# Optimization experiments

Hardware: AMD Instinct MI355X
Metric: run time of the kernel (lower is better)

The kernel has to match this reference:

```python
import jax, jax.numpy as jnp
import numpy as np

N, D_IN, D_OUT, E = 16384, 2048, 2048, 8


def setup_inputs() -> dict:
    key = jax.random.key(0)
    k1, k2, k3, k4 = jax.random.split(key, 4)
    x = jax.random.normal(k1, (N, D_IN), dtype=jnp.float32)
    idxs = jax.random.randint(k2, (N,), 0, E, dtype=jnp.int64)
    # nn.Linear params: weight [out, in], bias [out]; stacked over experts.
    W = jax.random.normal(k3, (E, D_OUT, D_IN), dtype=jnp.float32) * (1.0 / np.sqrt(D_IN))
    b = jax.random.normal(k4, (E, D_OUT), dtype=jnp.float32) * 0.01
    return {"x": x, "idxs": idxs, "W": W, "b": b}


def reference(x, idxs, W, b):
    # Hard-routed MoE: each token goes to exactly one expert's Linear, then ReLU.
    # Loop over the small fixed expert count; each iteration is one dense GEMM
    # over all tokens, combined with a per-token routing mask (equivalent math
    # to the original masked gather/scatter since every token matches exactly
    # one expert id in [0, E)).
    n_experts = W.shape[0]
    y = jnp.zeros((x.shape[0], W.shape[1]), dtype=x.dtype)
    for e in range(n_experts):
        mask = (idxs == e)[:, None]  # [N, 1]
        y_e = x @ W[e].T + b[e]      # [N, out]
        y = jnp.where(mask, y_e, y)
    return jax.nn.relu(y)
```

## Files before the change

kernel.cpp:

```cpp
#include <hip/hip_runtime.h>
#include <stdint.h>

#define N_TOK 16384
#define D_IN  2048
#define D_OUT 2048
#define NEXP  8

#define BM 128
#define BN 128
#define BK 32

typedef __attribute__((ext_vector_type(8))) short bf16x8;
typedef __attribute__((ext_vector_type(4))) float f32x4;
typedef __attribute__((ext_vector_type(4))) unsigned short u16x4;

static __device__ __forceinline__ unsigned short f2bf(float x) {
  unsigned u = __builtin_bit_cast(unsigned, x);
  u += 0x7FFFu + ((u >> 16) & 1u);
  return (unsigned short)(u >> 16);
}
static __device__ __forceinline__ float bf2f(unsigned short h) {
  unsigned u = ((unsigned)h) << 16;
  return __builtin_bit_cast(float, u);
}

__global__ void zero_cnt(int* cnt) {
  if (threadIdx.x < NEXP) cnt[threadIdx.x] = 0;
}

__global__ void route_kernel(const int* __restrict__ idxs, int* __restrict__ cnt,
                             int* __restrict__ bucket) {
  int t = blockIdx.x * blockDim.x + threadIdx.x;
  if (t < N_TOK) {
    int e = idxs[t];
    int slot = atomicAdd(&cnt[e], 1);
    bucket[e * N_TOK + slot] = t;
  }
}

__global__ void split_kernel(const float* __restrict__ in, unsigned short* __restrict__ hi,
                             unsigned short* __restrict__ lo, int n4) {
  int i = blockIdx.x * blockDim.x + threadIdx.x;
  int stride = gridDim.x * blockDim.x;
  const float4* in4 = (const float4*)in;
  for (; i < n4; i += stride) {
    float4 v = in4[i];
    float f[4] = {v.x, v.y, v.z, v.w};
    u16x4 h, l;
#pragma unroll
    for (int j = 0; j < 4; ++j) {
      unsigned short hh = f2bf(f[j]);
      h[j] = hh;
      l[j] = f2bf(f[j] - bf2f(hh));
    }
    *(u16x4*)(hi + (size_t)i * 4) = h;
    *(u16x4*)(lo + (size_t)i * 4) = l;
  }
}

#define GLD16(g, l)                                                                       \
  __builtin_amdgcn_global_load_lds((const __attribute__((address_space(1))) void*)(g),    \
                                   (__attribute__((address_space(3))) void*)(l), 16, 0, 0)

__global__ __launch_bounds__(256)
void moe_gemm(const unsigned short* __restrict__ xhi, const unsigned short* __restrict__ xlo,
              const unsigned short* __restrict__ whi, const unsigned short* __restrict__ wlo,
              const float* __restrict__ bias, const int* __restrict__ cnt,
              const int* __restrict__ bucket, float* __restrict__ out) {
  const int e = blockIdx.z;
  const int count = cnt[e];
  const int m0 = blockIdx.y * BM;
  if (m0 >= count) return;
  const int n0 = blockIdx.x * BN;

  __shared__ __align__(16) unsigned short sAh[BM * BK];
  __shared__ __align__(16) unsigned short sAl[BM * BK];
  __shared__ __align__(16) unsigned short sBh[BN * BK];
  __shared__ __align__(16) unsigned short sBl[BN * BK];
  __shared__ int rowtok[BM];

  const int tid = threadIdx.x;
  const int lane = tid & 63;
  const int wave = tid >> 6;

  if (tid < BM) {
    int r = m0 + tid;
    rowtok[tid] = bucket[e * N_TOK + (r < count ? r : count - 1)];
  }
  __syncthreads();

  const int s0 = tid;
  const int s1 = 256 + tid;
  const int row0 = s0 >> 2, seg0 = s0 & 3;
  const int row1 = s1 >> 2, seg1 = s1 & 3;
  const int tok0 = rowtok[row0];
  const int tok1 = rowtok[row1];
  const size_t aOff0 = (size_t)tok0 * D_IN + seg0 * 8;
  const size_t aOff1 = (size_t)tok1 * D_IN + seg1 * 8;
  const size_t bOff0 = (size_t)(n0 + row0) * D_IN + seg0 * 8;
  const size_t bOff1 = (size_t)(n0 + row1) * D_IN + seg1 * 8;
  const unsigned short* wBh = whi + (size_t)e * D_OUT * D_IN;
  const unsigned short* wBl = wlo + (size_t)e * D_OUT * D_IN;
  const int lb0 = wave * 1024;
  const int lb1 = 4096 + wave * 1024;

  f32x4 acc[4][4];
#pragma unroll
  for (int i = 0; i < 4; ++i)
#pragma unroll
    for (int j = 0; j < 4; ++j) acc[i][j] = (f32x4)0.0f;

  const int r16 = lane & 15;
  const int ko = (lane >> 4) * 8;
  const int wm = (wave >> 1) * 64;
  const int wn = (wave & 1) * 64;

  for (int kt = 0; kt < D_IN; kt += BK) {
    __syncthreads();
    GLD16(xhi + aOff0 + kt, (char*)sAh + lb0);
    GLD16(xhi + aOff1 + kt, (char*)sAh + lb1);
    GLD16(xlo + aOff0 + kt, (char*)sAl + lb0);
    GLD16(xlo + aOff1 + kt, (char*)sAl + lb1);
    GLD16(wBh + bOff0 + kt, (char*)sBh + lb0);
    GLD16(wBh + bOff1 + kt, (char*)sBh + lb1);
    GLD16(wBl + bOff0 + kt, (char*)sBl + lb0);
    GLD16(wBl + bOff1 + kt, (char*)sBl + lb1);
    __syncthreads();

    bf16x8 ah[4], al[4], bh[4], bl[4];
#pragma unroll
    for (int i = 0; i < 4; ++i) {
      ah[i] = *(const bf16x8*)&sAh[(wm + i * 16 + r16) * BK + ko];
      al[i] = *(const bf16x8*)&sAl[(wm + i * 16 + r16) * BK + ko];
      bh[i] = *(const bf16x8*)&sBh[(wn + i * 16 + r16) * BK + ko];
      bl[i] = *(const bf16x8*)&sBl[(wn + i * 16 + r16) * BK + ko];
    }
#pragma unroll
    for (int mi = 0; mi < 4; ++mi)
#pragma unroll
      for (int ni = 0; ni < 4; ++ni) {
        acc[mi][ni] = __builtin_amdgcn_mfma_f32_16x16x32_bf16(ah[mi], bh[ni], acc[mi][ni], 0, 0, 0);
        acc[mi][ni] = __builtin_amdgcn_mfma_f32_16x16x32_bf16(ah[mi], bl[ni], acc[mi][ni], 0, 0, 0);
        acc[mi][ni] = __builtin_amdgcn_mfma_f32_16x16x32_bf16(al[mi], bh[ni], acc[mi][ni], 0, 0, 0);
      }
  }

  const int rbase = (lane >> 4) * 4;
#pragma unroll
  for (int ni = 0; ni < 4; ++ni) {
    const int gn = n0 + wn + ni * 16 + r16;
    const float bv = bias[e * D_OUT + gn];
#pragma unroll
    for (int mi = 0; mi < 4; ++mi) {
#pragma unroll
      for (int i = 0; i < 4; ++i) {
        const int lr = wm + mi * 16 + rbase + i;
        if (m0 + lr < count) {
          const int tok = rowtok[lr];
          out[(size_t)tok * D_OUT + gn] = fmaxf(acc[mi][ni][i] + bv, 0.0f);
        }
      }
    }
  }
}

__global__ void fallback_kernel(const float* __restrict__ x, const int* __restrict__ idxs,
                                const float* __restrict__ W, const float* __restrict__ b,
                                float* __restrict__ out) {
  const int row = blockIdx.y;
  const int col = blockIdx.x * 256 + threadIdx.x;
  const int e = idxs[row];
  const float4* xr = (const float4*)(x + (size_t)row * D_IN);
  const float4* wr = (const float4*)(W + ((size_t)e * D_OUT + col) * D_IN);
  float acc = 0.f;
  for (int k = 0; k < D_IN / 4; ++k) {
    float4 a = xr[k], w = wr[k];
    acc += a.x * w.x + a.y * w.y + a.z * w.z + a.w * w.w;
  }
  out[(size_t)row * D_OUT + col] = fmaxf(acc + b[e * D_OUT + col], 0.0f);
}

extern "C" void kernel_launch(void* const* d_in, const int* in_sizes, int n_in,
                              void* d_out, int out_size, void* d_ws, size_t ws_size,
                              hipStream_t stream) {
  const float* x = (const float*)d_in[0];
  const int* idxs = (const int*)d_in[1];
  const float* W = (const float*)d_in[2];
  const float* b = (const float*)d_in[3];
  float* out = (float*)d_out;

  size_t off = 0;
  auto alloc = [&](size_t bytes) {
    void* p = (char*)d_ws + off;
    off += (bytes + 255) & ~(size_t)255;
    return p;
  };
  int* cnt = (int*)alloc(NEXP * sizeof(int));
  int* bucket = (int*)alloc((size_t)NEXP * N_TOK * sizeof(int));
  unsigned short* xhi = (unsigned short*)alloc((size_t)N_TOK * D_IN * 2);
  unsigned short* xlo = (unsigned short*)alloc((size_t)N_TOK * D_IN * 2);
  unsigned short* whi = (unsigned short*)alloc((size_t)NEXP * D_OUT * D_IN * 2);
  unsigned short* wlo = (unsigned short*)alloc((size_t)NEXP * D_OUT * D_IN * 2);

  if (off > ws_size) {
    dim3 g(D_OUT / 256, N_TOK, 1);
    fallback_kernel<<<g, 256, 0, stream>>>(x, idxs, W, b, out);
    return;
  }

  zero_cnt<<<1, 64, 0, stream>>>(cnt);
  route_kernel<<<(N_TOK + 255) / 256, 256, 0, stream>>>(idxs, cnt, bucket);

  const int n4x = N_TOK * D_IN / 4;
  const int n4w = NEXP * D_OUT * D_IN / 4;
  split_kernel<<<2048, 256, 0, stream>>>(x, xhi, xlo, n4x);
  split_kernel<<<2048, 256, 0, stream>>>(W, whi, wlo, n4w);

  dim3 grid(D_OUT / BN, (N_TOK + BM - 1) / BM, NEXP);
  moe_gemm<<<grid, 256, 0, stream>>>(xhi, xlo, whi, wlo, b, cnt, bucket, out);
}
```

Measured before the change: 931.5 us.

## Use 256x256 tiles with double-buffered swizzled LDS and interleaved MFMA scheduling

The grouped GEMM moves to 256x256 tiles on 8 waves, with a double-buffered 64KB-per-stage LDS ring. Global-to-LDS loads for the next K step are interleaved with four MFMA phases, separated by scheduling barriers and priority hints. An XOR swizzle on the LDS layout avoids bank conflicts, and the routing kernel now uses shared-memory histograms to cut global atomics. The larger tiles raise operand reuse and overlap memory with compute, at the cost of more padding waste per expert and lower occupancy from the 128KB of LDS per block.

Result: faster. 847.2 us (-9.0%).

```diff
diff --git a/kernel.cpp b/kernel.cpp
--- a/kernel.cpp
+++ b/kernel.cpp
@@ -6,9 +6,10 @@
 #define D_OUT 2048
 #define NEXP  8
 
-#define BM 128
-#define BN 128
+#define BM 256
+#define BN 256
 #define BK 32
+#define NKT (D_IN / BK)
 
 typedef __attribute__((ext_vector_type(8))) short bf16x8;
 typedef __attribute__((ext_vector_type(4))) float f32x4;
@@ -30,12 +31,20 @@
 
 __global__ void route_kernel(const int* __restrict__ idxs, int* __restrict__ cnt,
                              int* __restrict__ bucket) {
-  int t = blockIdx.x * blockDim.x + threadIdx.x;
-  if (t < N_TOK) {
-    int e = idxs[t];
-    int slot = atomicAdd(&cnt[e], 1);
-    bucket[e * N_TOK + slot] = t;
-  }
+  __shared__ int hist[NEXP];
+  __shared__ int base[NEXP];
+  __shared__ int pos[NEXP];
+  const int t = blockIdx.x * 256 + threadIdx.x;
+  if (threadIdx.x < NEXP) { hist[threadIdx.x] = 0; pos[threadIdx.x] = 0; }
+  __syncthreads();
+  const int e = idxs[t];
+  atomicAdd(&hist[e], 1);
+  __syncthreads();
+  if (threadIdx.x < NEXP)
+    base[threadIdx.x] = atomicAdd(&cnt[threadIdx.x], hist[threadIdx.x]);
+  __syncthreads();
+  const int r = atomicAdd(&pos[e], 1);
+  bucket[e * N_TOK + base[e] + r] = t;
 }
 
 __global__ void split_kernel(const float* __restrict__ in, unsigned short* __restrict__ hi,
@@ -58,11 +67,50 @@
   }
 }
 
-#define GLD16(g, l)                                                                       \
-  __builtin_amdgcn_global_load_lds((const __attribute__((address_space(1))) void*)(g),    \
+#define GLD16(g, l)                                                                    \
+  __builtin_amdgcn_global_load_lds((const __attribute__((address_space(1))) void*)(g), \
                                    (__attribute__((address_space(3))) void*)(l), 16, 0, 0)
-
-__global__ __launch_bounds__(256)
+#define SB() __builtin_amdgcn_sched_barrier(0)
+#define BAR() __builtin_amdgcn_s_barrier()
+
+template <int MH>
+static __device__ __forceinline__ void loadA(const char* rb, int wr, int off0,
+                                             bf16x8 (&afr)[4][2]) {
+#pragma unroll
+  for (int mf = 0; mf < 4; ++mf) {
+    const int ro = (wr * 128 + MH * 64 + mf * 16) * 128;
+    afr[mf][0] = *(const bf16x8*)(rb + ro + off0);
+    afr[mf][1] = *(const bf16x8*)(rb + ro + (off0 ^ 64));
+  }
+}
+
+template <int NH>
+static __device__ __forceinline__ void loadB(const char* rb, int wc, int off0,
+                                             bf16x8 (&bfr)[2][2]) {
+#pragma unroll
+  for (int nf = 0; nf < 2; ++nf) {
+    const int ro = 32768 + (wc * 64 + NH * 32 + nf * 16) * 128;
+    bfr[nf][0] = *(const bf16x8*)(rb + ro + off0);
+    bfr[nf][1] = *(const bf16x8*)(rb + ro + (off0 ^ 64));
+  }
+}
+
+template <int MH, int NH>
+static __device__ __forceinline__ void mfma24(bf16x8 (&afr)[4][2], bf16x8 (&bfr)[2][2],
+                                              f32x4 (&acc)[8][4]) {
+#pragma unroll
+  for (int mf = 0; mf < 4; ++mf)
+#pragma unroll
+    for (int nf = 0; nf < 2; ++nf) {
+      f32x4 a = acc[MH * 4 + mf][NH * 2 + nf];
+      a = __builtin_amdgcn_mfma_f32_16x16x32_bf16(afr[mf][0], bfr[nf][0], a, 0, 0, 0);
+      a = __builtin_amdgcn_mfma_f32_16x16x32_bf16(afr[mf][0], bfr[nf][1], a, 0, 0, 0);
+      a = __builtin_amdgcn_mfma_f32_16x16x32_bf16(afr[mf][1], bfr[nf][0], a, 0, 0, 0);
+      acc[MH * 4 + mf][NH * 2 + nf] = a;
+    }
+}
+
+__global__ __launch_bounds__(512, 2)
 void moe_gemm(const unsigned short* __restrict__ xhi, const unsigned short* __restrict__ xlo,
               const unsigned short* __restrict__ whi, const unsigned short* __restrict__ wlo,
               const float* __restrict__ bias, const int* __restrict__ cnt,
@@ -73,15 +121,14 @@
   if (m0 >= count) return;
   const int n0 = blockIdx.x * BN;
 
-  __shared__ __align__(16) unsigned short sAh[BM * BK];
-  __shared__ __align__(16) unsigned short sAl[BM * BK];
-  __shared__ __align__(16) unsigned short sBh[BN * BK];
-  __shared__ __align__(16) unsigned short sBl[BN * BK];
+  __shared__ __align__(16) char sbuf[2][65536];
   __shared__ int rowtok[BM];
 
   const int tid = threadIdx.x;
   const int lane = tid & 63;
-  const int wave = tid >> 6;
+  const int w = tid >> 6;
+  const int wr = w >> 2;
+  const int wc = w & 3;
 
   if (tid < BM) {
     int r = m0 + tid;
@@ -89,75 +136,90 @@
   }
   __syncthreads();
 
-  const int s0 = tid;
-  const int s1 = 256 + tid;
-  const int row0 = s0 >> 2, seg0 = s0 & 3;
-  const int row1 = s1 >> 2, seg1 = s1 & 3;
-  const int tok0 = rowtok[row0];
-  const int tok1 = rowtok[row1];
-  const size_t aOff0 = (size_t)tok0 * D_IN + seg0 * 8;
-  const size_t aOff1 = (size_t)tok1 * D_IN + seg1 * 8;
-  const size_t bOff0 = (size_t)(n0 + row0) * D_IN + seg0 * 8;
-  const size_t bOff1 = (size_t)(n0 + row1) * D_IN + seg1 * 8;
-  const unsigned short* wBh = whi + (size_t)e * D_OUT * D_IN;
-  const unsigned short* wBl = wlo + (size_t)e * D_OUT * D_IN;
-  const int lb0 = wave * 1024;
-  const int lb1 = 4096 + wave * 1024;
-
-  f32x4 acc[4][4];
-#pragma unroll
-  for (int i = 0; i < 4; ++i)
+  const unsigned short* whiE = whi + (size_t)e * D_OUT * D_IN;
+  const unsigned short* wloE = wlo + (size_t)e * D_OUT * D_IN;
+  const unsigned short* srcb[8];
+#pragma unroll
+  for (int q = 0; q < 8; ++q) {
+    const int r = (q & 3) * 64 + (tid >> 3);
+    const int c = (tid & 7) ^ ((tid >> 3) & 7);
+    const int half = c >> 2, kc = c & 3;
+    if (q < 4) {
+      const int tok = rowtok[r];
+      srcb[q] = (half ? xlo : xhi) + (size_t)tok * D_IN + kc * 8;
+    } else {
+      srcb[q] = (half ? wloE : whiE) + (size_t)(n0 + r) * D_IN + kc * 8;
+    }
+  }
+  const int dstoff = w * 1024;
+
+  const int off0 = (lane & 15) * 128 + (((lane >> 4) ^ (lane & 7)) * 16);
+
+  f32x4 acc[8][4];
+#pragma unroll
+  for (int i = 0; i < 8; ++i)
 #pragma unroll
     for (int j = 0; j < 4; ++j) acc[i][j] = (f32x4)0.0f;
+  bf16x8 afr[4][2], bfr[2][2];
+
+  {
+    char* wb = sbuf[0];
+#pragma unroll
+    for (int q = 0; q < 8; ++q) GLD16(srcb[q], wb + q * 8192 + dstoff);
+  }
+  asm volatile("s_waitcnt vmcnt(0)" ::: "memory");
+  SB(); BAR(); SB();
+
+  int cur = 0;
+  for (int i = 0; i < NKT; ++i) {
+    const char* rb = sbuf[cur];
+    char* wb = sbuf[cur ^ 1];
+    const int ktn = (i + 1) * BK;
+    const bool nx = (i + 1 < NKT);
+
+    loadA<0>(rb, wr, off0, afr);
+    loadB<0>(rb, wc, off0, bfr);
+    if (nx) { GLD16(srcb[0] + ktn, wb + 0 * 8192 + dstoff); GLD16(srcb[1] + ktn, wb + 1 * 8192 + dstoff); }
+    SB(); BAR(); SB();
+    __builtin_amdgcn_s_setprio(1); mfma24<0, 0>(afr, bfr, acc); __builtin_amdgcn_s_setprio(0);
+    SB(); BAR(); SB();
+
+    loadB<1>(rb, wc, off0, bfr);
+    if (nx) { GLD16(srcb[2] + ktn, wb + 2 * 8192 + dstoff); GLD16(srcb[3] + ktn, wb + 3 * 8192 + dstoff); }
+    SB(); BAR(); SB();
+    __builtin_amdgcn_s_setprio(1); mfma24<0, 1>(afr, bfr, acc); __builtin_amdgcn_s_setprio(0);
+    SB(); BAR(); SB();
+
+    loadA<1>(rb, wr, off0, afr);
+    loadB<0>(rb, wc, off0, bfr);
+    if (nx) { GLD16(srcb[4] + ktn, wb + 4 * 8192 + dstoff); GLD16(srcb[5] + ktn, wb + 5 * 8192 + dstoff); }
+    SB(); BAR(); SB();
+    __builtin_amdgcn_s_setprio(1); mfma24<1, 0>(afr, bfr, acc); __builtin_amdgcn_s_setprio(0);
+    SB(); BAR(); SB();
+
+    loadB<1>(rb, wc, off0, bfr);
+    if (nx) { GLD16(srcb[6] + ktn, wb + 6 * 8192 + dstoff); GLD16(srcb[7] + ktn, wb + 7 * 8192 + dstoff); }
+    SB(); BAR(); SB();
+    __builtin_amdgcn_s_setprio(1); mfma24<1, 1>(afr, bfr, acc); __builtin_amdgcn_s_setprio(0);
+    asm volatile("s_waitcnt vmcnt(0)" ::: "memory");
+    SB(); BAR(); SB();
+    cur ^= 1;
+  }
 
   const int r16 = lane & 15;
-  const int ko = (lane >> 4) * 8;
-  const int wm = (wave >> 1) * 64;
-  const int wn = (wave & 1) * 64;
-
-  for (int kt = 0; kt < D_IN; kt += BK) {
-    __syncthreads();
-    GLD16(xhi + aOff0 + kt, (char*)sAh + lb0);
-    GLD16(xhi + aOff1 + kt, (char*)sAh + lb1);
-    GLD16(xlo + aOff0 + kt, (char*)sAl + lb0);
-    GLD16(xlo + aOff1 + kt, (char*)sAl + lb1);
-    GLD16(wBh + bOff0 + kt, (char*)sBh + lb0);
-    GLD16(wBh + bOff1 + kt, (char*)sBh + lb1);
-    GLD16(wBl + bOff0 + kt, (char*)sBl + lb0);
-    GLD16(wBl + bOff1 + kt, (char*)sBl + lb1);
-    __syncthreads();
-
-    bf16x8 ah[4], al[4], bh[4], bl[4];
-#pragma unroll
-    for (int i = 0; i < 4; ++i) {
-      ah[i] = *(const bf16x8*)&sAh[(wm + i * 16 + r16) * BK + ko];
-      al[i] = *(const bf16x8*)&sAl[(wm + i * 16 + r16) * BK + ko];
-      bh[i] = *(const bf16x8*)&sBh[(wn + i * 16 + r16) * BK + ko];
-      bl[i] = *(const bf16x8*)&sBl[(wn + i * 16 + r16) * BK + ko];
-    }
-#pragma unroll
-    for (int mi = 0; mi < 4; ++mi)
-#pragma unroll
-      for (int ni = 0; ni < 4; ++ni) {
-        acc[mi][ni] = __builtin_amdgcn_mfma_f32_16x16x32_bf16(ah[mi], bh[ni], acc[mi][ni], 0, 0, 0);
-        acc[mi][ni] = __builtin_amdgcn_mfma_f32_16x16x32_bf16(ah[mi], bl[ni], acc[mi][ni], 0, 0, 0);
-        acc[mi][ni] = __builtin_amdgcn_mfma_f32_16x16x32_bf16(al[mi], bh[ni], acc[mi][ni], 0, 0, 0);
-      }
-  }
-
-  const int rbase = (lane >> 4) * 4;
-#pragma unroll
-  for (int ni = 0; ni < 4; ++ni) {
-    const int gn = n0 + wn + ni * 16 + r16;
+  const int rb4 = (lane >> 4) * 4;
+#pragma unroll
+  for (int n = 0; n < 4; ++n) {
+    const int gn = n0 + wc * 64 + n * 16 + r16;
     const float bv = bias[e * D_OUT + gn];
 #pragma unroll
-    for (int mi = 0; mi < 4; ++mi) {
-#pragma unroll
-      for (int i = 0; i < 4; ++i) {
-        const int lr = wm + mi * 16 + rbase + i;
-        if (m0 + lr < count) {
-          const int tok = rowtok[lr];
-          out[(size_t)tok * D_OUT + gn] = fmaxf(acc[mi][ni][i] + bv, 0.0f);
+    for (int m = 0; m < 8; ++m) {
+      const int lr = wr * 128 + m * 16 + rb4;
+#pragma unroll
+      for (int i2 = 0; i2 < 4; ++i2) {
+        const int row = lr + i2;
+        if (m0 + row < count) {
+          out[(size_t)rowtok[row] * D_OUT + gn] = fmaxf(acc[m][n][i2] + bv, 0.0f);
         }
       }
     }
@@ -209,13 +271,13 @@
   }
 
   zero_cnt<<<1, 64, 0, stream>>>(cnt);
-  route_kernel<<<(N_TOK + 255) / 256, 256, 0, stream>>>(idxs, cnt, bucket);
+  route_kernel<<<N_TOK / 256, 256, 0, stream>>>(idxs, cnt, bucket);
 
   const int n4x = N_TOK * D_IN / 4;
   const int n4w = NEXP * D_OUT * D_IN / 4;
   split_kernel<<<2048, 256, 0, stream>>>(x, xhi, xlo, n4x);
   split_kernel<<<2048, 256, 0, stream>>>(W, whi, wlo, n4w);
 
-  dim3 grid(D_OUT / BN, (N_TOK + BM - 1) / BM, NEXP);
-  moe_gemm<<<grid, 256, 0, stream>>>(xhi, xlo, whi, wlo, b, cnt, bucket, out);
-}
+  dim3 grid(D_OUT / BN, N_TOK / BM, NEXP);
+  moe_gemm<<<grid, 512, 0, stream>>>(xhi, xlo, whi, wlo, b, cnt, bucket, out);
+}
```
